# Optimization experiments

Hardware: AMD Instinct MI355X
Metric: run time of the kernel (lower is better)

Reference implementation:

```python
import jax, jax.numpy as jnp
import numpy as np

D_MODEL = 768
N_HEADS = 12
D_HEAD = 64
WINDOW = 16
LOOK_BACK = 1
IGNORE = -1.0e6


def look_around(x, backward=LOOK_BACK, forward=0, pad_value=0):
    # x: (b, n_windows, w, ...) -> (b, n_windows, w*(backward+forward+1), ...)
    n = x.shape[1]
    pad = [(0, 0)] * x.ndim
    pad[1] = (backward, forward)
    px = jnp.pad(x, pad, constant_values=pad_value)
    return jnp.concatenate([px[:, i:i + n] for i in range(backward + forward + 1)], axis=2)


def setup_inputs() -> dict:
    key = jax.random.key(0)
    k1, k2, k3 = jax.random.split(key, 3)
    B, T = 2, 2048
    x = jax.random.normal(k1, (B, T, D_MODEL), dtype=jnp.float32)
    W_abcde = jax.random.normal(k2, (D_MODEL, 5 * N_HEADS * D_HEAD), dtype=jnp.float32) * (1.0 / np.sqrt(D_MODEL))
    b_abcde = jnp.zeros((5 * N_HEADS * D_HEAD,), dtype=jnp.float32)
    W_O = jax.random.normal(k3, (N_HEADS * D_HEAD, D_MODEL), dtype=jnp.float32) * (1.0 / np.sqrt(N_HEADS * D_HEAD))
    b_O = jnp.zeros((D_MODEL,), dtype=jnp.float32)
    return {"x": x, "W_abcde": W_abcde, "b_abcde": b_abcde, "W_O": W_O, "b_O": b_O}


def reference(x, W_abcde, b_abcde, W_O, b_O):
    B, T, _ = x.shape
    w = WINDOW
    nw = T // w
    Ww = w * (LOOK_BACK + 1)  # look-around window length

    abcde = x @ W_abcde + b_abcde                                    # (B,T,5*H*D)
    abcde = abcde.reshape(B, T, 5, N_HEADS, D_HEAD).transpose(2, 0, 3, 1, 4)  # (5,B,H,T,D)
    a, b, c, d, e = [t.reshape(B * N_HEADS, nw, w, D_HEAD) for t in abcde]
    a_l, b_l, d_l, e_l = (look_around(t) for t in (a, b, d, e))       # (BH,nw,Ww,D)

    # causal mask, same construction as get_causal_mask (pad_value=0)
    seq = jnp.arange(T).reshape(1, nw, w)
    bb = look_around(seq)                                            # (1,nw,Ww)
    # mask[n,m,l] = (seq_n < bb_l) | (bb_l <= bb_m)
    mask = (seq[..., :, None, None] < bb[..., None, None, :]) | (bb[..., None, None, :] <= bb[..., None, :, None])

    # third-order attention scores: (BH, nw, w, Ww, Ww)
    scores = jnp.einsum('bnwd,bnmd,bnld->bnwml', c, a_l, b_l)
    scores = jnp.where(mask, IGNORE, scores)
    scores = jnp.where(scores == 0, IGNORE, scores)
    probs = jax.nn.softmax((scores / D_HEAD).reshape(B * N_HEADS, nw, w, Ww * Ww), axis=-1)
    probs = probs.reshape(scores.shape)

    z = jnp.einsum('bnwml,bnmd->bnwd', probs, d_l) + jnp.einsum('bnwml,bnld->bnwd', probs, e_l)
    z = z.reshape(B, N_HEADS, nw, w, D_HEAD).transpose(0, 2, 3, 1, 4).reshape(B, T, N_HEADS * D_HEAD)
    return z @ W_O + b_O
```

## Files before the change

kernel.cpp:

```cpp
#include <hip/hip_runtime.h>

#define T_SEQ   2048
#define NHEADS  12
#define DHEAD   64
#define WIN     16
#define WW      32
#define NWIN    128
#define DMODEL  768
#define NABCDE  3840
#define IGNORE_V (-1.0e6f)
#define PAD_K   72
#define L2E64   0.022542110013890053f
#define IGN_SC  (-22542.110013890053f)

typedef float f32x4 __attribute__((ext_vector_type(4)));
typedef _Float16 f16x8 __attribute__((ext_vector_type(8)));

__device__ __forceinline__ short f2h(float f) {
    union { _Float16 h; short s; } u;
    u.h = (_Float16)f;
    return u.s;
}

__device__ __forceinline__ void gload_lds16(const short* g, short* l) {
    __builtin_amdgcn_global_load_lds(
        (const __attribute__((address_space(1))) void*)g,
        (__attribute__((address_space(3))) void*)l,
        16, 0, 0);
}

__global__ __launch_bounds__(256) void prep_kernel(
    const float* __restrict__ x, const float* __restrict__ W_abcde,
    const float* __restrict__ W_O,
    short* __restrict__ xh, short* __restrict__ Wt, short* __restrict__ WOt)
{
    __shared__ float tile[32][33];
    const int blk = blockIdx.x;
    const int tid = threadIdx.x;

    if (blk < 1536) {
        int i = (blk * 256 + tid) * 8;
        float4 a = *reinterpret_cast<const float4*>(&x[i]);
        float4 b = *reinterpret_cast<const float4*>(&x[i + 4]);
        union { short s[8]; uint4 u; } r;
        r.s[0] = f2h(a.x); r.s[1] = f2h(a.y); r.s[2] = f2h(a.z); r.s[3] = f2h(a.w);
        r.s[4] = f2h(b.x); r.s[5] = f2h(b.y); r.s[6] = f2h(b.z); r.s[7] = f2h(b.w);
        *reinterpret_cast<uint4*>(&xh[i]) = r.u;
        return;
    }
    const float* W; short* Wo; int N, bx, by;
    if (blk < 4416) {
        int t = blk - 1536;
        W = W_abcde; Wo = Wt; N = NABCDE;
        bx = (t % 120) * 32; by = (t / 120) * 32;
    } else {
        int t = blk - 4416;
        W = W_O; Wo = WOt; N = DMODEL;
        bx = (t % 24) * 32; by = (t / 24) * 32;
    }
    const int tx = tid & 31, ty = tid >> 5;
#pragma unroll
    for (int r = 0; r < 32; r += 8)
        tile[ty + r][tx] = W[(size_t)(by + ty + r) * N + bx + tx];
    __syncthreads();
#pragma unroll
    for (int r = 0; r < 32; r += 8)
        Wo[(size_t)(bx + ty + r) * DMODEL + by + tx] = f2h(tile[tx][ty + r]);
}

__global__ __launch_bounds__(512, 2) void gemm1_kernel(
    const short* __restrict__ A, const short* __restrict__ Bt,
    const float* __restrict__ bias, short* __restrict__ C,
    int M, int N, int K)
{
    __shared__ short LT[4][2][8192];

    const int tid  = threadIdx.x;
    const int wave = tid >> 6;
    const int lane = tid & 63;

    int bid = blockIdx.x;
    int t = (bid & 7) * 30 + (bid >> 3);
    const int bm = (t / 15) * 256;
    const int bn = (t % 15) * 256;

    const int wr = wave >> 2;
    const int wc = wave & 3;
    const int fm = lane & 15;
    const int ko = lane >> 4;
    const int kswz = ko ^ ((lane >> 2) & 3);
    const int w32 = wave * 32;

    const int srow = lane >> 2;
    const int scc  = ((lane & 3) ^ ((lane >> 4) & 3)) * 8;
    const short* gA[2]; const short* gB[2];
#pragma unroll
    for (int j = 0; j < 2; ++j) {
        gA[j] = A  + (size_t)(bm + w32 + j * 16 + srow) * K + scc;
        gB[j] = Bt + (size_t)(bn + w32 + j * 16 + srow) * K + scc;
    }

    f32x4 acc[8][4];
#pragma unroll
    for (int mi = 0; mi < 8; ++mi)
#pragma unroll
        for (int ni = 0; ni < 4; ++ni) acc[mi][ni] = (f32x4){0.f, 0.f, 0.f, 0.f};

#pragma unroll
    for (int kt = 0; kt < 3; ++kt) {
#pragma unroll
        for (int j = 0; j < 2; ++j) {
            gload_lds16(gA[j] + kt * 32, &LT[kt][0][(w32 + j * 16) * 32]);
            gload_lds16(gB[j] + kt * 32, &LT[kt][1][(w32 + j * 16) * 32]);
        }
    }

    const int NKT = K >> 5;
    const int nkm = NKT - 3;

#define G1_STEP(KB, VMC, DOSTAGE, KS)                                          \
    {                                                                          \
        asm volatile("s_waitcnt vmcnt(" #VMC ")" ::: "memory");                \
        __builtin_amdgcn_s_barrier();                                          \
        asm volatile("" ::: "memory");                                         \
        if (DOSTAGE) {                                                         \
            int sb_ = (KS) & 3;                                                \
            _Pragma("unroll")                                                  \
            for (int j = 0; j < 2; ++j) {                                      \
                gload_lds16(gA[j] + (KS) * 32, &LT[sb_][0][(w32 + j * 16) * 32]); \
                gload_lds16(gB[j] + (KS) * 32, &LT[sb_][1][(w32 + j * 16) * 32]); \
            }                                                                  \
        }                                                                      \
        const short* Ab_ = &LT[(KB)][0][0];                                    \
        const short* Bb_ = &LT[(KB)][1][0];                                    \
        f16x8 af_[8], bf_[4];                                                  \
        _Pragma("unroll")                                                      \
        for (int mi = 0; mi < 8; ++mi)                                         \
            af_[mi] = *reinterpret_cast<const f16x8*>(                         \
                &Ab_[(wr * 128 + mi * 16 + fm) * 32 + kswz * 8]);              \
        _Pragma("unroll")                                                      \
        for (int ni = 0; ni < 4; ++ni)                                         \
            bf_[ni] = *reinterpret_cast<const f16x8*>(                         \
                &Bb_[(wc * 64 + ni * 16 + fm) * 32 + kswz * 8]);               \
        __builtin_amdgcn_s_setprio(1);                                         \
        _Pragma("unroll")                                                      \
        for (int mi = 0; mi < 8; ++mi)                                         \
            _Pragma("unroll")                                                  \
            for (int ni = 0; ni < 4; ++ni)                                     \
                acc[mi][ni] = __builtin_amdgcn_mfma_f32_16x16x32_f16(          \
                    af_[mi], bf_[ni], acc[mi][ni], 0, 0, 0);                   \
        __builtin_amdgcn_s_setprio(0);                                         \
    }

    for (int k = 0; k < nkm; ++k) {
        G1_STEP(k & 3, 8, true, k + 3);
    }
    G1_STEP(nkm & 3, 8, false, 0);
    G1_STEP((nkm + 1) & 3, 4, false, 0);
    G1_STEP((nkm + 2) & 3, 0, false, 0);
#undef G1_STEP

    float bv[4];
#pragma unroll
    for (int ni = 0; ni < 4; ++ni)
        bv[ni] = bias[bn + wc * 64 + ni * 16 + fm];

    short* cb = &LT[0][0][0];
#pragma unroll
    for (int half = 0; half < 2; ++half) {
        __syncthreads();
        if (wr == half) {
#pragma unroll
            for (int mi = 0; mi < 8; ++mi) {
#pragma unroll
                for (int r = 0; r < 4; ++r) {
                    int lrow = mi * 16 + ko * 4 + r;
#pragma unroll
                    for (int ni = 0; ni < 4; ++ni)
                        cb[lrow * 256 + wc * 64 + ni * 16 + fm] =
                            f2h(acc[mi][ni][r] + bv[ni]);
                }
            }
        }
        __syncthreads();
#pragma unroll
        for (int q = 0; q < 8; ++q) {
            int f = tid + q * 512;
            int row = f >> 5, c16 = (f & 31) * 8;
            *reinterpret_cast<uint4*>(
                &C[(size_t)(bm + half * 128 + row) * N + bn + c16]) =
                *reinterpret_cast<const uint4*>(&cb[row * 256 + c16]);
        }
    }
}

__global__ __launch_bounds__(256) void gemm_h16_64(
    const short* __restrict__ A, const short* __restrict__ Bt,
    const float* __restrict__ bias, float* __restrict__ C,
    int M, int N, int K)
{
    __shared__ short As[2][64 * 32];
    __shared__ short Bs[2][64 * 32];

    const int tid  = threadIdx.x;
    const int wave = tid >> 6;
    const int lane = tid & 63;
    const int bm = blockIdx.y * 64;
    const int bn = blockIdx.x * 64;

    const int st_row = lane >> 2;
    const int st_col = (lane & 3) * 8;
    const int fr_m = lane & 15;
    const int fr_k = (lane >> 4) * 8;
    const int wm = wave * 16;

    const short* gsrc[4];
    short* ldst[4];
#pragma unroll
    for (int j = 0; j < 4; ++j) {
        int c = wave * 4 + j;
        if (c < 8) {
            int kt = c >> 2, rg = c & 3;
            gsrc[j] = A + (size_t)(bm + rg * 16 + st_row) * K + kt * 32 + st_col;
            ldst[j] = &As[kt][(rg * 16) * 32];
        } else {
            int cb = c - 8;
            int kt = cb >> 2, rg = cb & 3;
            gsrc[j] = Bt + (size_t)(bn + rg * 16 + st_row) * K + kt * 32 + st_col;
            ldst[j] = &Bs[kt][(rg * 16) * 32];
        }
    }

    f32x4 acc[4];
#pragma unroll
    for (int ni = 0; ni < 4; ++ni) acc[ni] = (f32x4){0.f, 0.f, 0.f, 0.f};

    for (int k0 = 0; k0 < K; k0 += 64) {
#pragma unroll
        for (int j = 0; j < 4; ++j) gload_lds16(gsrc[j] + k0, ldst[j]);
        __syncthreads();

#pragma unroll
        for (int kt = 0; kt < 2; ++kt) {
            f16x8 af = *reinterpret_cast<const f16x8*>(
                &As[kt][(wm + fr_m) * 32 + fr_k]);
#pragma unroll
            for (int ni = 0; ni < 4; ++ni) {
                f16x8 bf = *reinterpret_cast<const f16x8*>(
                    &Bs[kt][(ni * 16 + fr_m) * 32 + fr_k]);
                acc[ni] = __builtin_amdgcn_mfma_f32_16x16x32_f16(
                    af, bf, acc[ni], 0, 0, 0);
            }
        }
        __syncthreads();
    }

    float bv[4];
#pragma unroll
    for (int ni = 0; ni < 4; ++ni)
        bv[ni] = bias[bn + ni * 16 + (lane & 15)];
    int rbase = bm + wm + (lane >> 4) * 4;
#pragma unroll
    for (int r = 0; r < 4; ++r) {
        size_t off = (size_t)(rbase + r) * N + bn + (lane & 15);
#pragma unroll
        for (int ni = 0; ni < 4; ++ni)
            C[off + ni * 16] = acc[ni][r] + bv[ni];
    }
}

__global__ __launch_bounds__(256) void attn_kernel(
    const short* __restrict__ abcde, short* __restrict__ z)
{
    const int bid = blockIdx.x;
    const int blk = (bid & 7) * 384 + (bid >> 3);
    const int n  = blk & (NWIN - 1);
    const int bh = blk >> 7;
    const int b  = bh / NHEADS;
    const int h  = bh % NHEADS;

    __shared__ short sc[WIN * PAD_K];
    __shared__ short sa[WW * PAD_K];
    __shared__ short sb[WW * PAD_K];
    __shared__ short sd[WW * PAD_K];
    __shared__ short se[WW * PAD_K];
    __shared__ short epA[WIN * PAD_K];
    __shared__ float sinv[WIN];

    const int tid = threadIdx.x;
    const size_t rowbase = ((size_t)b * T_SEQ) * NABCDE;
    const int hd = h * DHEAD;

    if (tid < 128) {
        int row = tid >> 3, ch = (tid & 7) * 8;
        *reinterpret_cast<uint4*>(&sc[row * PAD_K + ch]) =
            *reinterpret_cast<const uint4*>(
                &abcde[rowbase + (size_t)(n * WIN + row) * NABCDE + 2 * DMODEL + hd + ch]);
    }
    {
        int row = tid >> 3, ch = (tid & 7) * 8;
        int t = n * WIN - WIN + row;
        uint4 va = {0u, 0u, 0u, 0u}, vb = va, vd = va, ve = va;
        if (t >= 0) {
            size_t base = rowbase + (size_t)t * NABCDE + hd + ch;
            va = *reinterpret_cast<const uint4*>(&abcde[base + 0 * DMODEL]);
            vb = *reinterpret_cast<const uint4*>(&abcde[base + 1 * DMODEL]);
            vd = *reinterpret_cast<const uint4*>(&abcde[base + 3 * DMODEL]);
            ve = *reinterpret_cast<const uint4*>(&abcde[base + 4 * DMODEL]);
        }
        *reinterpret_cast<uint4*>(&sa[row * PAD_K + ch]) = va;
        *reinterpret_cast<uint4*>(&sb[row * PAD_K + ch]) = vb;
        *reinterpret_cast<uint4*>(&sd[row * PAD_K + ch]) = vd;
        *reinterpret_cast<uint4*>(&se[row * PAD_K + ch]) = ve;
    }
    __syncthreads();

    const int wv = tid >> 6;
    const int lane = tid & 63;
    const int lc = lane & 15;
    const int ko = lane >> 4;

    f16x8 cfrag[2];
    f16x8 bfrag[2][2];
#pragma unroll
    for (int kt = 0; kt < 2; ++kt) {
        cfrag[kt] = *reinterpret_cast<const f16x8*>(
            &sc[(wv * 4 + (lc & 3)) * PAD_K + kt * 32 + ko * 8]) * (_Float16)L2E64;
        bfrag[0][kt] = *reinterpret_cast<const f16x8*>(&sb[lc * PAD_K + kt * 32 + ko * 8]);
        bfrag[1][kt] = *reinterpret_cast<const f16x8*>(&sb[(16 + lc) * PAD_K + kt * 32 + ko * 8]);
    }

    f32x4 acc[8][2];
#pragma unroll
    for (int mt = 0; mt < 8; ++mt) {
        acc[mt][0] = (f32x4){0.f, 0.f, 0.f, 0.f};
        acc[mt][1] = (f32x4){0.f, 0.f, 0.f, 0.f};
    }
    __builtin_amdgcn_s_setprio(1);
#pragma unroll
    for (int mt = 0; mt < 8; ++mt) {
#pragma unroll
        for (int kt = 0; kt < 2; ++kt) {
            f16x8 ar = *reinterpret_cast<const f16x8*>(
                &sa[(mt * 4 + (lc >> 2)) * PAD_K + kt * 32 + ko * 8]);
            f16x8 pa = cfrag[kt] * ar;
            acc[mt][0] = __builtin_amdgcn_mfma_f32_16x16x32_f16(pa, bfrag[0][kt], acc[mt][0], 0, 0, 0);
            acc[mt][1] = __builtin_amdgcn_mfma_f32_16x16x32_f16(pa, bfrag[1][kt], acc[mt][1], 0, 0, 0);
        }
    }
    __builtin_amdgcn_s_setprio(0);

    const int nbase = n * WIN;
    if (n != 0) {
#pragma unroll
        for (int lt = 0; lt < 2; ++lt) {
            const int l = lt * 16 + lc;
#pragma unroll
            for (int mt = 0; mt < 8; ++mt) {
                const bool mgt = l > (mt * 4 + ko);
#pragma unroll
                for (int reg = 0; reg < 4; ++reg) {
                    const bool keep = mgt && (wv * 4 + reg + WIN >= l);
                    float p = __builtin_amdgcn_exp2f(acc[mt][lt][reg]);
                    acc[mt][lt][reg] = keep ? p : 0.0f;
                }
            }
        }
    } else {
        int bbl_h[2]; bool keepL[2][4];
#pragma unroll
        for (int lt = 0; lt < 2; ++lt) {
            int l = lt * 16 + lc;
            bbl_h[lt] = (l < WIN) ? 0 : (l - WIN);
#pragma unroll
            for (int reg = 0; reg < 4; ++reg)
                keepL[lt][reg] = (wv * 4 + reg) >= bbl_h[lt];
        }
#pragma unroll
        for (int mt = 0; mt < 8; ++mt) {
            int m = mt * 4 + ko;
            int bbm = (m < WIN) ? 0 : (m - WIN);
#pragma unroll
            for (int lt = 0; lt < 2; ++lt) {
                bool mgt = bbl_h[lt] > bbm;
#pragma unroll
                for (int reg = 0; reg < 4; ++reg) {
                    float s = acc[mt][lt][reg];
                    if (!(keepL[lt][reg] && mgt) || s == 0.0f)
                        acc[mt][lt][reg] = IGN_SC;
                }
            }
        }
        float mx[4] = {-3.4e38f, -3.4e38f, -3.4e38f, -3.4e38f};
#pragma unroll
        for (int mt = 0; mt < 8; ++mt)
#pragma unroll
            for (int lt = 0; lt < 2; ++lt)
#pragma unroll
                for (int reg = 0; reg < 4; ++reg)
                    mx[reg] = fmaxf(mx[reg], acc[mt][lt][reg]);
#pragma unroll
        for (int reg = 0; reg < 4; ++reg) {
#pragma unroll
            for (int off = 1; off < 64; off <<= 1)
                mx[reg] = fmaxf(mx[reg], __shfl_xor(mx[reg], off, 64));
        }
#pragma unroll
        for (int mt = 0; mt < 8; ++mt)
#pragma unroll
            for (int lt = 0; lt < 2; ++lt)
#pragma unroll
                for (int reg = 0; reg < 4; ++reg)
                    acc[mt][lt][reg] = __builtin_amdgcn_exp2f(
                        acc[mt][lt][reg] - mx[reg]);
    }

    float plv[2][4];
#pragma unroll
    for (int lt = 0; lt < 2; ++lt) {
#pragma unroll
        for (int reg = 0; reg < 4; ++reg) {
            float p = acc[0][lt][reg];
#pragma unroll
            for (int mt = 1; mt < 8; ++mt) p += acc[mt][lt][reg];
            p += __shfl_xor(p, 16, 64);
            p += __shfl_xor(p, 32, 64);
            plv[lt][reg] = p;
        }
        float w  = (ko & 1) ? plv[lt][1] : plv[lt][0];
        float w2 = (ko & 1) ? plv[lt][3] : plv[lt][2];
        float ww = (ko & 2) ? w2 : w;
        epA[(wv * 4 + ko) * PAD_K + 32 + lt * 16 + lc] = f2h(ww);
    }

    {
        float s[4];
#pragma unroll
        for (int reg = 0; reg < 4; ++reg) {
            float t = plv[0][reg] + plv[1][reg];
            t += __shfl_xor(t, 1, 64);
            t += __shfl_xor(t, 2, 64);
            t += __shfl_xor(t, 4, 64);
            t += __shfl_xor(t, 8, 64);
            s[reg] = t;
        }
        if (lane == 0) {
#pragma unroll
            for (int reg = 0; reg < 4; ++reg) sinv[wv * 4 + reg] = 1.0f / s[reg];
        }
    }

    {
        float v8[8][4];
#pragma unroll
        for (int mt = 0; mt < 8; ++mt)
#pragma unroll
            for (int reg = 0; reg < 4; ++reg)
                v8[mt][reg] = acc[mt][0][reg] + acc[mt][1][reg];

        const bool s0 = lane & 1, s1 = lane & 2, s2 = lane & 4, s3 = lane & 8;
        float r1[4][4];
#pragma unroll
        for (int m2 = 0; m2 < 4; ++m2)
#pragma unroll
            for (int reg = 0; reg < 4; ++reg) {
                float u = v8[2 * m2][reg], w = v8[2 * m2 + 1][reg];
                float a = s0 ? w : u;
                float s = s0 ? u : w;
                r1[m2][reg] = a + __shfl_xor(s, 1, 64);
            }
        float r2[2][4];
#pragma unroll
        for (int m4 = 0; m4 < 2; ++m4)
#pragma unroll
            for (int reg = 0; reg < 4; ++reg) {
                float u = r1[2 * m4][reg], w = r1[2 * m4 + 1][reg];
                float a = s1 ? w : u;
                float s = s1 ? u : w;
                r2[m4][reg] = a + __shfl_xor(s, 2, 64);
            }
        float r3[4];
#pragma unroll
        for (int reg = 0; reg < 4; ++reg) {
            float u = r2[0][reg], w = r2[1][reg];
            float a = s2 ? w : u;
            float s = s2 ? u : w;
            r3[reg] = a + __shfl_xor(s, 4, 64);
        }
        float a0 = s3 ? r3[1] : r3[0];
        float q0 = s3 ? r3[0] : r3[1];
        float g0 = a0 + __shfl_xor(q0, 8, 64);
        float a1 = s3 ? r3[3] : r3[2];
        float q1 = s3 ? r3[2] : r3[3];
        float g1 = a1 + __shfl_xor(q1, 8, 64);

        int mcol = (lc & 7) * 4 + ko;
        int ib = wv * 4 + (lc >> 3);
        epA[ib * PAD_K + mcol]       = f2h(g0);
        epA[(ib + 2) * PAD_K + mcol] = f2h(g1);
    }

    const int dd = wv * 16 + lc;
    f16x8 bd, be;
    {
        unsigned dv[8], ev[8];
#pragma unroll
        for (int j = 0; j < 8; ++j) {
            dv[j] = *reinterpret_cast<const unsigned short*>(&sd[(ko * 8 + j) * PAD_K + dd]);
            ev[j] = *reinterpret_cast<const unsigned short*>(&se[(ko * 8 + j) * PAD_K + dd]);
        }
        union { unsigned u[4]; f16x8 v; } td, te;
#pragma unroll
        for (int j = 0; j < 4; ++j) {
            td.u[j] = __builtin_amdgcn_perm(dv[2 * j + 1], dv[2 * j], 0x05040100);
            te.u[j] = __builtin_amdgcn_perm(ev[2 * j + 1], ev[2 * j], 0x05040100);
        }
        bd = td.v; be = te.v;
    }
    __syncthreads();

    f16x8 apm = *reinterpret_cast<const f16x8*>(&epA[lc * PAD_K + ko * 8]);
    f16x8 apl = *reinterpret_cast<const f16x8*>(&epA[lc * PAD_K + 32 + ko * 8]);
    f32x4 zacc = (f32x4){0.f, 0.f, 0.f, 0.f};
    __builtin_amdgcn_s_setprio(1);
    zacc = __builtin_amdgcn_mfma_f32_16x16x32_f16(apm, bd, zacc, 0, 0, 0);
    zacc = __builtin_amdgcn_mfma_f32_16x16x32_f16(apl, be, zacc, 0, 0, 0);
    __builtin_amdgcn_s_setprio(0);

    short* zs = sd;
#pragma unroll
    for (int reg = 0; reg < 4; ++reg) {
        int i = ko * 4 + reg;
        zs[i * 64 + dd] = f2h(zacc[reg] * sinv[i]);
    }
    __syncthreads();
    {
        int row = tid >> 4;
        int ch  = (tid & 15) * 4;
        *reinterpret_cast<uint2*>(
            &z[((size_t)b * T_SEQ + nbase + row) * (NHEADS * DHEAD) + hd + ch]) =
            *reinterpret_cast<const uint2*>(&zs[row * 64 + ch]);
    }
}

extern "C" void kernel_launch(void* const* d_in, const int* in_sizes, int n_in,
                              void* d_out, int out_size, void* d_ws, size_t ws_size,
                              hipStream_t stream) {
    const float* x        = (const float*)d_in[0];
    const float* W_abcde  = (const float*)d_in[1];
    const float* b_abcde  = (const float*)d_in[2];
    const float* W_O      = (const float*)d_in[3];
    const float* b_O      = (const float*)d_in[4];
    float* out = (float*)d_out;

    char* ws = (char*)d_ws;
    short* abcde = (short*)ws;
    short* xh    = (short*)(ws + (size_t)31457280);
    short* Wt    = (short*)(ws + (size_t)31457280 + 6291456);
    short* WOt   = (short*)(ws + (size_t)31457280 + 6291456 + 5898240);
    short* zb    = xh;

    const int M = 2 * T_SEQ;

    prep_kernel<<<dim3(4992), dim3(256), 0, stream>>>(
        x, W_abcde, W_O, xh, Wt, WOt);

    gemm1_kernel<<<dim3(240), dim3(512), 0, stream>>>(
        xh, Wt, b_abcde, abcde, M, NABCDE, DMODEL);

    attn_kernel<<<dim3(2 * NHEADS * NWIN), dim3(256), 0, stream>>>(abcde, zb);

    gemm_h16_64<<<dim3(DMODEL / 64, M / 64), dim3(256), 0, stream>>>(
        zb, WOt, b_O, out, M, DMODEL, DMODEL);
}
```

Before: 145.8 us.

## Process two adjacent windows per attention block to share look-around loads

The attention kernel now handles two consecutive windows per 512-thread block instead of one window per 256-thread block, halving the grid. The overlapping look-around rows of a, b, d and e are loaded into shared memory once (48 rows instead of 2×32), which cuts redundant global loads and per-block launch overhead. In exchange, each block uses more shared memory and fewer blocks are launched, which may reduce occupancy or load balance.

```diff
diff --git a/kernel.cpp b/kernel.cpp
--- a/kernel.cpp
+++ b/kernel.cpp
@@ -269,37 +269,38 @@
     }
 }
 
-__global__ __launch_bounds__(256) void attn_kernel(
+__global__ __launch_bounds__(512) void attn_kernel(
     const short* __restrict__ abcde, short* __restrict__ z)
 {
     const int bid = blockIdx.x;
-    const int blk = (bid & 7) * 384 + (bid >> 3);
-    const int n  = blk & (NWIN - 1);
-    const int bh = blk >> 7;
+    const int blk = (bid & 7) * 192 + (bid >> 3);
+    const int jp = blk & 63;
+    const int bh = blk >> 6;
     const int b  = bh / NHEADS;
     const int h  = bh % NHEADS;
-
-    __shared__ short sc[WIN * PAD_K];
-    __shared__ short sa[WW * PAD_K];
-    __shared__ short sb[WW * PAD_K];
-    __shared__ short sd[WW * PAD_K];
-    __shared__ short se[WW * PAD_K];
-    __shared__ short epA[WIN * PAD_K];
-    __shared__ float sinv[WIN];
+    const int n0 = jp * 2;
+
+    __shared__ short sc[32 * PAD_K];
+    __shared__ short sa[48 * PAD_K];
+    __shared__ short sb[48 * PAD_K];
+    __shared__ short sd[48 * PAD_K];
+    __shared__ short se[48 * PAD_K];
+    __shared__ short epA[32 * PAD_K];
+    __shared__ float sinv[32];
 
     const int tid = threadIdx.x;
     const size_t rowbase = ((size_t)b * T_SEQ) * NABCDE;
     const int hd = h * DHEAD;
 
-    if (tid < 128) {
+    if (tid < 256) {
         int row = tid >> 3, ch = (tid & 7) * 8;
         *reinterpret_cast<uint4*>(&sc[row * PAD_K + ch]) =
             *reinterpret_cast<const uint4*>(
-                &abcde[rowbase + (size_t)(n * WIN + row) * NABCDE + 2 * DMODEL + hd + ch]);
-    }
-    {
+                &abcde[rowbase + (size_t)(n0 * WIN + row) * NABCDE + 2 * DMODEL + hd + ch]);
+    }
+    if (tid < 384) {
         int row = tid >> 3, ch = (tid & 7) * 8;
-        int t = n * WIN - WIN + row;
+        int t = n0 * WIN - WIN + row;
         uint4 va = {0u, 0u, 0u, 0u}, vb = va, vd = va, ve = va;
         if (t >= 0) {
             size_t base = rowbase + (size_t)t * NABCDE + hd + ch;
@@ -316,18 +317,23 @@
     __syncthreads();
 
     const int wv = tid >> 6;
+    const int w  = wv >> 2;
+    const int wvl = wv & 3;
+    const int n  = n0 + w;
     const int lane = tid & 63;
     const int lc = lane & 15;
     const int ko = lane >> 4;
+    const int lb = w * 16;
+    const int ew = w * 16;
 
     f16x8 cfrag[2];
     f16x8 bfrag[2][2];
 #pragma unroll
     for (int kt = 0; kt < 2; ++kt) {
         cfrag[kt] = *reinterpret_cast<const f16x8*>(
-            &sc[(wv * 4 + (lc & 3)) * PAD_K + kt * 32 + ko * 8]) * (_Float16)L2E64;
-        bfrag[0][kt] = *reinterpret_cast<const f16x8*>(&sb[lc * PAD_K + kt * 32 + ko * 8]);
-        bfrag[1][kt] = *reinterpret_cast<const f16x8*>(&sb[(16 + lc) * PAD_K + kt * 32 + ko * 8]);
+            &sc[(ew + wvl * 4 + (lc & 3)) * PAD_K + kt * 32 + ko * 8]) * (_Float16)L2E64;
+        bfrag[0][kt] = *reinterpret_cast<const f16x8*>(&sb[(lb + lc) * PAD_K + kt * 32 + ko * 8]);
+        bfrag[1][kt] = *reinterpret_cast<const f16x8*>(&sb[(lb + 16 + lc) * PAD_K + kt * 32 + ko * 8]);
     }
 
     f32x4 acc[8][2];
@@ -342,7 +348,7 @@
 #pragma unroll
         for (int kt = 0; kt < 2; ++kt) {
             f16x8 ar = *reinterpret_cast<const f16x8*>(
-                &sa[(mt * 4 + (lc >> 2)) * PAD_K + kt * 32 + ko * 8]);
+                &sa[(lb + mt * 4 + (lc >> 2)) * PAD_K + kt * 32 + ko * 8]);
             f16x8 pa = cfrag[kt] * ar;
             acc[mt][0] = __builtin_amdgcn_mfma_f32_16x16x32_f16(pa, bfrag[0][kt], acc[mt][0], 0, 0, 0);
             acc[mt][1] = __builtin_amdgcn_mfma_f32_16x16x32_f16(pa, bfrag[1][kt], acc[mt][1], 0, 0, 0);
@@ -350,7 +356,6 @@
     }
     __builtin_amdgcn_s_setprio(0);
 
-    const int nbase = n * WIN;
     if (n != 0) {
 #pragma unroll
         for (int lt = 0; lt < 2; ++lt) {
@@ -360,7 +365,7 @@
                 const bool mgt = l > (mt * 4 + ko);
 #pragma unroll
                 for (int reg = 0; reg < 4; ++reg) {
-                    const bool keep = mgt && (wv * 4 + reg + WIN >= l);
+                    const bool keep = mgt && (wvl * 4 + reg + WIN >= l);
                     float p = __builtin_amdgcn_exp2f(acc[mt][lt][reg]);
                     acc[mt][lt][reg] = keep ? p : 0.0f;
                 }
@@ -374,7 +379,7 @@
             bbl_h[lt] = (l < WIN) ? 0 : (l - WIN);
 #pragma unroll
             for (int reg = 0; reg < 4; ++reg)
-                keepL[lt][reg] = (wv * 4 + reg) >= bbl_h[lt];
+                keepL[lt][reg] = (wvl * 4 + reg) >= bbl_h[lt];
         }
 #pragma unroll
         for (int mt = 0; mt < 8; ++mt) {
@@ -427,10 +432,10 @@
             p += __shfl_xor(p, 32, 64);
             plv[lt][reg] = p;
         }
-        float w  = (ko & 1) ? plv[lt][1] : plv[lt][0];
+        float w1  = (ko & 1) ? plv[lt][1] : plv[lt][0];
         float w2 = (ko & 1) ? plv[lt][3] : plv[lt][2];
-        float ww = (ko & 2) ? w2 : w;
-        epA[(wv * 4 + ko) * PAD_K + 32 + lt * 16 + lc] = f2h(ww);
+        float ww = (ko & 2) ? w2 : w1;
+        epA[(ew + wvl * 4 + ko) * PAD_K + 32 + lt * 16 + lc] = f2h(ww);
     }
 
     {
@@ -446,7 +451,7 @@
         }
         if (lane == 0) {
 #pragma unroll
-            for (int reg = 0; reg < 4; ++reg) sinv[wv * 4 + reg] = 1.0f / s[reg];
+            for (int reg = 0; reg < 4; ++reg) sinv[ew + wvl * 4 + reg] = 1.0f / s[reg];
         }
     }
 
@@ -464,9 +469,9 @@
         for (int m2 = 0; m2 < 4; ++m2)
 #pragma unroll
             for (int reg = 0; reg < 4; ++reg) {
-                float u = v8[2 * m2][reg], w = v8[2 * m2 + 1][reg];
-                float a = s0 ? w : u;
-                float s = s0 ? u : w;
+                float u = v8[2 * m2][reg], wq = v8[2 * m2 + 1][reg];
+                float a = s0 ? wq : u;
+                float s = s0 ? u : wq;
                 r1[m2][reg] = a + __shfl_xor(s, 1, 64);
             }
         float r2[2][4];
@@ -474,17 +479,17 @@
         for (int m4 = 0; m4 < 2; ++m4)
 #pragma unroll
             for (int reg = 0; reg < 4; ++reg) {
-                float u = r1[2 * m4][reg], w = r1[2 * m4 + 1][reg];
-                float a = s1 ? w : u;
-                float s = s1 ? u : w;
+                float u = r1[2 * m4][reg], wq = r1[2 * m4 + 1][reg];
+                float a = s1 ? wq : u;
+                float s = s1 ? u : wq;
                 r2[m4][reg] = a + __shfl_xor(s, 2, 64);
             }
         float r3[4];
 #pragma unroll
         for (int reg = 0; reg < 4; ++reg) {
-            float u = r2[0][reg], w = r2[1][reg];
-            float a = s2 ? w : u;
-            float s = s2 ? u : w;
+            float u = r2[0][reg], wq = r2[1][reg];
+            float a = s2 ? wq : u;
+            float s = s2 ? u : wq;
             r3[reg] = a + __shfl_xor(s, 4, 64);
         }
         float a0 = s3 ? r3[1] : r3[0];
@@ -495,19 +500,19 @@
         float g1 = a1 + __shfl_xor(q1, 8, 64);
 
         int mcol = (lc & 7) * 4 + ko;
-        int ib = wv * 4 + (lc >> 3);
+        int ib = ew + wvl * 4 + (lc >> 3);
         epA[ib * PAD_K + mcol]       = f2h(g0);
         epA[(ib + 2) * PAD_K + mcol] = f2h(g1);
     }
 
-    const int dd = wv * 16 + lc;
+    const int dd = wvl * 16 + lc;
     f16x8 bd, be;
     {
         unsigned dv[8], ev[8];
 #pragma unroll
         for (int j = 0; j < 8; ++j) {
-            dv[j] = *reinterpret_cast<const unsigned short*>(&sd[(ko * 8 + j) * PAD_K + dd]);
-            ev[j] = *reinterpret_cast<const unsigned short*>(&se[(ko * 8 + j) * PAD_K + dd]);
+            dv[j] = *reinterpret_cast<const unsigned short*>(&sd[(lb + ko * 8 + j) * PAD_K + dd]);
+            ev[j] = *reinterpret_cast<const unsigned short*>(&se[(lb + ko * 8 + j) * PAD_K + dd]);
         }
         union { unsigned u[4]; f16x8 v; } td, te;
 #pragma unroll
@@ -519,8 +524,8 @@
     }
     __syncthreads();
 
-    f16x8 apm = *reinterpret_cast<const f16x8*>(&epA[lc * PAD_K + ko * 8]);
-    f16x8 apl = *reinterpret_cast<const f16x8*>(&epA[lc * PAD_K + 32 + ko * 8]);
+    f16x8 apm = *reinterpret_cast<const f16x8*>(&epA[(ew + lc) * PAD_K + ko * 8]);
+    f16x8 apl = *reinterpret_cast<const f16x8*>(&epA[(ew + lc) * PAD_K + 32 + ko * 8]);
     f32x4 zacc = (f32x4){0.f, 0.f, 0.f, 0.f};
     __builtin_amdgcn_s_setprio(1);
     zacc = __builtin_amdgcn_mfma_f32_16x16x32_f16(apm, bd, zacc, 0, 0, 0);
@@ -530,7 +535,7 @@
     short* zs = sd;
 #pragma unroll
     for (int reg = 0; reg < 4; ++reg) {
-        int i = ko * 4 + reg;
+        int i = ew + ko * 4 + reg;
         zs[i * 64 + dd] = f2h(zacc[reg] * sinv[i]);
     }
     __syncthreads();
@@ -538,7 +543,7 @@
         int row = tid >> 4;
         int ch  = (tid & 15) * 4;
         *reinterpret_cast<uint2*>(
-            &z[((size_t)b * T_SEQ + nbase + row) * (NHEADS * DHEAD) + hd + ch]) =
+            &z[((size_t)b * T_SEQ + n0 * WIN + row) * (NHEADS * DHEAD) + hd + ch]) =
             *reinterpret_cast<const uint2*>(&zs[row * 64 + ch]);
     }
 }
@@ -568,7 +573,7 @@
     gemm1_kernel<<<dim3(240), dim3(512), 0, stream>>>(
         xh, Wt, b_abcde, abcde, M, NABCDE, DMODEL);
 
-    attn_kernel<<<dim3(2 * NHEADS * NWIN), dim3(256), 0, stream>>>(abcde, zb);
+    attn_kernel<<<dim3(NHEADS * NWIN), dim3(512), 0, stream>>>(abcde, zb);
 
     gemm_h16_64<<<dim3(DMODEL / 64, M / 64), dim3(256), 0, stream>>>(
         zb, WOt, b_O, out, M, DMODEL, DMODEL);
```

New measurement: 146.1 us. No clear change (+0.3%).
